# Performance work log

Measured on AMD Instinct MI355X. Metric: run time of the kernel, lower is better.

Reference implementation:

```python
import jax, jax.numpy as jnp
import numpy as np

NEG_SLOPE = 0.2  # PyG GATConv default leaky_relu slope


def gat_layer(x, src, dst, W, a_src, a_dst, bias, heads, d, concat):
    # x: [N, in_dim]; src/dst: [E] (edges flow src -> dst, self-loops included)
    N = x.shape[0]
    h = (x @ W).reshape(N, heads, d)                      # [N, H, D]
    alpha_src = jnp.einsum('nhd,hd->nh', h, a_src)        # [N, H]
    alpha_dst = jnp.einsum('nhd,hd->nh', h, a_dst)        # [N, H]
    e = jax.nn.leaky_relu(alpha_src[src] + alpha_dst[dst], NEG_SLOPE)  # [E, H]
    # softmax over incoming edges of each destination node (segment softmax)
    m = jax.ops.segment_max(e, dst, num_segments=N)       # [N, H]
    ex = jnp.exp(e - m[dst])
    s = jax.ops.segment_sum(ex, dst, num_segments=N)      # [N, H]
    alpha = ex / s[dst]                                   # [E, H]
    msg = h[src] * alpha[..., None]                       # [E, H, D]
    out = jax.ops.segment_sum(msg, dst, num_segments=N)   # [N, H, D]
    out = out.reshape(N, heads * d) if concat else out.mean(axis=1)
    return out + bias


def setup_inputs() -> dict:
    key = jax.random.key(0)
    ks = jax.random.split(key, 12)
    N, E = 10000, 320000
    in_dim, hidden, heads, out_dim = 256, 64, 4, 40
    x = jax.random.normal(ks[0], (N, in_dim), dtype=jnp.float32)
    edge_index = jax.random.randint(ks[1], (2, E), 0, N, dtype=jnp.int64)
    s = 0.1
    return {
        'x': x,
        'edge_index': edge_index,
        'W1': jax.random.normal(ks[2], (in_dim, heads * hidden), jnp.float32) * s,
        'att_src1': jax.random.normal(ks[3], (heads, hidden), jnp.float32) * s,
        'att_dst1': jax.random.normal(ks[4], (heads, hidden), jnp.float32) * s,
        'bias1': jnp.zeros((heads * hidden,), jnp.float32),
        'W2': jax.random.normal(ks[5], (heads * hidden, out_dim), jnp.float32) * s,
        'att_src2': jax.random.normal(ks[6], (1, out_dim), jnp.float32) * s,
        'att_dst2': jax.random.normal(ks[7], (1, out_dim), jnp.float32) * s,
        'bias2': jnp.zeros((out_dim,), jnp.float32),
    }


def reference(x, edge_index, W1, att_src1, att_dst1, bias1, W2, att_src2, att_dst2, bias2):
    N = x.shape[0]
    # PyG GATConv adds self-loops by default
    loop = jnp.arange(N, dtype=edge_index.dtype)
    src = jnp.concatenate([edge_index[0], loop])
    dst = jnp.concatenate([edge_index[1], loop])
    h = gat_layer(x, src, dst, W1, att_src1, att_dst1, bias1, heads=4, d=64, concat=True)
    h = jax.nn.relu(h)
    out = gat_layer(h, src, dst, W2, att_src2, att_dst2, bias2, heads=1, d=40, concat=False)
    return jax.nn.log_softmax(out, axis=1)
```

## Files before the change

kernel.cpp:

```cpp
#include <hip/hip_runtime.h>
#include <hip/hip_bf16.h>
#include <math.h>

#define IN_DIM 256
#define C1 256
#define H1 4
#define OUT_DIM 40
#define W2PAD 48
#define NEG_SLOPE 0.2f
#define DSTRIDE 128

typedef __attribute__((ext_vector_type(8))) short bf16x8;
typedef __attribute__((ext_vector_type(4))) float f32x4;
typedef __attribute__((ext_vector_type(2))) float f32x2;

#define XS_LD 264

__device__ __forceinline__ unsigned short f2bf(float f) {
    union { float f; unsigned u; } c; c.f = f;
    unsigned r = c.u + 0x7fffu + ((c.u >> 16) & 1u);
    return (unsigned short)(r >> 16);
}

__device__ __forceinline__ unsigned char f2fp8(float f) {
    return (unsigned char)__builtin_amdgcn_cvt_pk_fp8_f32(f, 0.f, 0, false);
}

__device__ __forceinline__ float sel4(float4 v, int h) {
    float r = v.x;
    r = (h == 1) ? v.y : r;
    r = (h == 2) ? v.z : r;
    r = (h == 3) ? v.w : r;
    return r;
}

__device__ __forceinline__ float leaky(float v) {
    return (v >= 0.0f) ? v : NEG_SLOPE * v;
}

__global__ void k_prep(int* __restrict__ fill, const float* __restrict__ W1,
                       unsigned short* __restrict__ W1t, const float* __restrict__ W2,
                       unsigned short* __restrict__ W2t, const float* __restrict__ a_src2,
                       const float* __restrict__ a_dst2, float* __restrict__ w2s,
                       float* __restrict__ w2d, int N) {
    int t = threadIdx.x;
    int g = blockIdx.x * 256 + t;
    if (g < N) fill[g << 4] = 0;
    if (g < C1) {
        float s = 0.0f, d = 0.0f;
#pragma unroll
        for (int j = 0; j < OUT_DIM; ++j) {
            float w = W2[g * OUT_DIM + j];
            s += w * a_src2[j];
            d += w * a_dst2[j];
        }
        w2s[g] = s;
        w2d[g] = d;
    }
    if (g < W2PAD * C1) {
        int j = g >> 8, k = g & 255;
        W2t[g] = (j < OUT_DIM) ? f2bf(W2[k * OUT_DIM + j]) : 0;
    }
    __shared__ float s32[32][33];
    int b = blockIdx.x;
    int r0 = (b >> 3) * 32;
    int c0 = (b & 7) * 32;
    for (int i = t; i < 1024; i += 256) {
        int lr = i >> 5, lc = i & 31;
        s32[lr][lc] = W1[(r0 + lr) * 256 + c0 + lc];
    }
    __syncthreads();
    for (int i = t; i < 1024; i += 256) {
        int oc = i >> 5, ok = i & 31;
        W1t[(c0 + oc) * 256 + r0 + ok] = f2bf(s32[ok][oc]);
    }
}

__global__ void __launch_bounds__(256) k_fused1(
    const float* __restrict__ x, const unsigned short* __restrict__ W1t,
    const float* __restrict__ a_src, const float* __restrict__ a_dst,
    unsigned char* __restrict__ h1, float* __restrict__ as1, float* __restrict__ ad1,
    const int* __restrict__ ei, int* __restrict__ fill, unsigned short* __restrict__ srcs,
    int N, int E, int ET, int G1) {
    __shared__ unsigned short xs[64 * XS_LD];
    int t = threadIdx.x;

    if (blockIdx.x >= G1) {
        int eb = (blockIdx.x - G1) * 1024 + t;
#pragma unroll
        for (int k = 0; k < 4; ++k) {
            int e = eb + k * 256;
            if (e < ET) {
                int s, d;
                if (e < E) { s = ei[e]; d = ei[E + e]; }
                else       { s = e - E; d = s; }
                int pos = atomicAdd(&fill[d << 4], 1);
                srcs[(d << 7) + pos] = (unsigned short)s;
            }
        }
        return;
    }

    int n0 = blockIdx.x * 64;
    for (int i = t; i < 4096; i += 256) {
        int r = i >> 6, c4 = i & 63;
        int n = n0 + r;
        float4 v = (n < N) ? ((const float4*)x)[(size_t)n * 64 + c4]
                           : make_float4(0.f, 0.f, 0.f, 0.f);
        uint2 pk;
        pk.x = (unsigned)f2bf(v.x) | ((unsigned)f2bf(v.y) << 16);
        pk.y = (unsigned)f2bf(v.z) | ((unsigned)f2bf(v.w) << 16);
        *((uint2*)&xs[r * XS_LD + c4 * 4]) = pk;
    }
    __syncthreads();

    int wv = t >> 6, lane = t & 63;
    int quad = lane >> 4, ln = lane & 15;

    f32x4 acc[4][4];
#pragma unroll
    for (int mt = 0; mt < 4; ++mt)
#pragma unroll
        for (int nt = 0; nt < 4; ++nt) acc[mt][nt] = (f32x4){0.f, 0.f, 0.f, 0.f};

#pragma unroll
    for (int kb = 0; kb < 8; ++kb) {
        bf16x8 af[4], bfv[4];
#pragma unroll
        for (int mt = 0; mt < 4; ++mt)
            af[mt] = *((bf16x8*)&xs[(mt * 16 + ln) * XS_LD + kb * 32 + quad * 8]);
#pragma unroll
        for (int nt = 0; nt < 4; ++nt)
            bfv[nt] = *((const bf16x8*)(W1t + ((wv * 64 + nt * 16 + ln) * 256 + kb * 32 + quad * 8)));
#pragma unroll
        for (int mt = 0; mt < 4; ++mt)
#pragma unroll
            for (int nt = 0; nt < 4; ++nt)
                acc[mt][nt] = __builtin_amdgcn_mfma_f32_16x16x32_bf16(af[mt], bfv[nt], acc[mt][nt], 0, 0, 0);
    }

    float asv[4], adv[4];
#pragma unroll
    for (int nt = 0; nt < 4; ++nt) {
        int col = wv * 64 + nt * 16 + ln;
        asv[nt] = a_src[col];
        adv[nt] = a_dst[col];
    }
#pragma unroll
    for (int mt = 0; mt < 4; ++mt) {
        float ds[4] = {0.f, 0.f, 0.f, 0.f};
        float dd[4] = {0.f, 0.f, 0.f, 0.f};
#pragma unroll
        for (int nt = 0; nt < 4; ++nt) {
#pragma unroll
            for (int r = 0; r < 4; ++r) {
                float v = acc[mt][nt][r];
                ds[r] += v * asv[nt];
                dd[r] += v * adv[nt];
            }
        }
#pragma unroll
        for (int r = 0; r < 4; ++r) {
            float vs = ds[r], vd = dd[r];
#pragma unroll
            for (int o = 1; o < 16; o <<= 1) {
                vs += __shfl_xor(vs, o);
                vd += __shfl_xor(vd, o);
            }
            if (ln == 0) {
                int node = n0 + mt * 16 + quad * 4 + r;
                if (node < N) {
                    as1[node * H1 + wv] = vs;
                    ad1[node * H1 + wv] = vd;
                }
            }
        }
    }

    __syncthreads();
    unsigned char* bt = (unsigned char*)xs;
#pragma unroll
    for (int mt = 0; mt < 4; ++mt)
#pragma unroll
        for (int nt = 0; nt < 4; ++nt)
#pragma unroll
            for (int r = 0; r < 4; ++r)
                bt[(mt * 16 + quad * 4 + r) * 256 + wv * 64 + nt * 16 + ln] = f2fp8(acc[mt][nt][r]);
    __syncthreads();
    const uint4* bt4 = (const uint4*)bt;
    uint4* h14 = (uint4*)(h1 + (size_t)n0 * C1);
    for (int i = t; i < 1024; i += 256) {
        int row = i >> 4;
        if (n0 + row < N) h14[i] = bt4[i];
    }
}

__global__ void __launch_bounds__(256) k_node1(
    const int* __restrict__ fill, const unsigned short* __restrict__ srcs,
    const float* __restrict__ as1f, const float* __restrict__ ad1f,
    const unsigned char* __restrict__ h1, const float* __restrict__ bias1,
    const float* __restrict__ w2s, const float* __restrict__ w2d,
    const unsigned short* __restrict__ W2t, unsigned short* __restrict__ h2b,
    float* __restrict__ as2, float* __restrict__ ad2, int N) {
    int w = threadIdx.x >> 6, lane = threadIdx.x & 63;
    int n = blockIdx.x * 4 + w;
    bool valid = (n < N);
    __shared__ float4 es[4][64];
    __shared__ unsigned short Abuf[16 * 256];
    int half = lane >> 5, hl = lane & 31;
    int h8 = hl >> 3;
    int start = n << 7;
    int end = start + (valid ? fill[n << 4] : 0);
    const float4* as4 = (const float4*)as1f;
    float4 adn = valid ? ((const float4*)ad1f)[n] : make_float4(0.f, 0.f, 0.f, 0.f);
    const float* esw = (const float*)&es[w][0];

    float4 S4 = make_float4(0.f, 0.f, 0.f, 0.f);
    float acc[8];
#pragma unroll
    for (int k = 0; k < 8; ++k) acc[k] = 0.f;

    for (int c = start; c < end; c += 64) {
        int cnt = min(64, end - c);
        int idx = c + lane;
        int sreg = (idx < end) ? (int)srcs[idx] : 0;
        float4 exv = make_float4(0.f, 0.f, 0.f, 0.f);
        if (idx < end) {
            float4 a = as4[sreg];
            exv.x = __expf(leaky(a.x + adn.x));
            exv.y = __expf(leaky(a.y + adn.y));
            exv.z = __expf(leaky(a.z + adn.z));
            exv.w = __expf(leaky(a.w + adn.w));
        }
        S4.x += exv.x; S4.y += exv.y; S4.z += exv.z; S4.w += exv.w;
        es[w][lane] = exv;

        int i = 0;
        for (; i + 15 < cnt; i += 16) {
            int s[8]; float a[8]; uint2 r[8];
#pragma unroll
            for (int k = 0; k < 8; ++k) {
                int j = i + 2 * k + half;
                s[k] = __shfl(sreg, j);
                a[k] = esw[j * 4 + h8];
            }
#pragma unroll
            for (int k = 0; k < 8; ++k)
                r[k] = *((const uint2*)(h1 + (size_t)s[k] * C1) + hl);
#pragma unroll
            for (int k = 0; k < 8; ++k) {
                f32x2 lo0 = __builtin_amdgcn_cvt_pk_f32_fp8(r[k].x, false);
                f32x2 hi0 = __builtin_amdgcn_cvt_pk_f32_fp8(r[k].x, true);
                f32x2 lo1 = __builtin_amdgcn_cvt_pk_f32_fp8(r[k].y, false);
                f32x2 hi1 = __builtin_amdgcn_cvt_pk_f32_fp8(r[k].y, true);
                acc[0] += a[k] * lo0.x; acc[1] += a[k] * lo0.y;
                acc[2] += a[k] * hi0.x; acc[3] += a[k] * hi0.y;
                acc[4] += a[k] * lo1.x; acc[5] += a[k] * lo1.y;
                acc[6] += a[k] * hi1.x; acc[7] += a[k] * hi1.y;
            }
        }
        for (; i + 7 < cnt; i += 8) {
            int s[4]; float a[4]; uint2 r[4];
#pragma unroll
            for (int k = 0; k < 4; ++k) {
                int j = i + 2 * k + half;
                s[k] = __shfl(sreg, j);
                a[k] = esw[j * 4 + h8];
            }
#pragma unroll
            for (int k = 0; k < 4; ++k)
                r[k] = *((const uint2*)(h1 + (size_t)s[k] * C1) + hl);
#pragma unroll
            for (int k = 0; k < 4; ++k) {
                f32x2 lo0 = __builtin_amdgcn_cvt_pk_f32_fp8(r[k].x, false);
                f32x2 hi0 = __builtin_amdgcn_cvt_pk_f32_fp8(r[k].x, true);
                f32x2 lo1 = __builtin_amdgcn_cvt_pk_f32_fp8(r[k].y, false);
                f32x2 hi1 = __builtin_amdgcn_cvt_pk_f32_fp8(r[k].y, true);
                acc[0] += a[k] * lo0.x; acc[1] += a[k] * lo0.y;
                acc[2] += a[k] * hi0.x; acc[3] += a[k] * hi0.y;
                acc[4] += a[k] * lo1.x; acc[5] += a[k] * lo1.y;
                acc[6] += a[k] * hi1.x; acc[7] += a[k] * hi1.y;
            }
        }
        for (; i < cnt; i += 2) {
            int j = i + half;
            int s0 = __shfl(sreg, j);
            float a0 = esw[j * 4 + h8];
            uint2 r0 = *((const uint2*)(h1 + (size_t)s0 * C1) + hl);
            f32x2 lo0 = __builtin_amdgcn_cvt_pk_f32_fp8(r0.x, false);
            f32x2 hi0 = __builtin_amdgcn_cvt_pk_f32_fp8(r0.x, true);
            f32x2 lo1 = __builtin_amdgcn_cvt_pk_f32_fp8(r0.y, false);
            f32x2 hi1 = __builtin_amdgcn_cvt_pk_f32_fp8(r0.y, true);
            acc[0] += a0 * lo0.x; acc[1] += a0 * lo0.y;
            acc[2] += a0 * hi0.x; acc[3] += a0 * hi0.y;
            acc[4] += a0 * lo1.x; acc[5] += a0 * lo1.y;
            acc[6] += a0 * hi1.x; acc[7] += a0 * hi1.y;
        }
    }

#pragma unroll
    for (int k = 0; k < 8; ++k) acc[k] += __shfl_xor(acc[k], 32);

#pragma unroll
    for (int o = 32; o > 0; o >>= 1) {
        S4.x += __shfl_xor(S4.x, o);
        S4.y += __shfl_xor(S4.y, o);
        S4.z += __shfl_xor(S4.z, o);
        S4.w += __shfl_xor(S4.w, o);
    }
    float iS = 1.0f / sel4(S4, h8);
    float4 b0 = ((const float4*)bias1)[hl * 2];
    float4 b1 = ((const float4*)bias1)[hl * 2 + 1];
    float v0 = fmaxf(acc[0] * iS + b0.x, 0.f);
    float v1 = fmaxf(acc[1] * iS + b0.y, 0.f);
    float v2 = fmaxf(acc[2] * iS + b0.z, 0.f);
    float v3 = fmaxf(acc[3] * iS + b0.w, 0.f);
    float v4 = fmaxf(acc[4] * iS + b1.x, 0.f);
    float v5 = fmaxf(acc[5] * iS + b1.y, 0.f);
    float v6 = fmaxf(acc[6] * iS + b1.z, 0.f);
    float v7 = fmaxf(acc[7] * iS + b1.w, 0.f);
    if (half == 0) {
        uint4 pk;
        pk.x = (unsigned)f2bf(v0) | ((unsigned)f2bf(v1) << 16);
        pk.y = (unsigned)f2bf(v2) | ((unsigned)f2bf(v3) << 16);
        pk.z = (unsigned)f2bf(v4) | ((unsigned)f2bf(v5) << 16);
        pk.w = (unsigned)f2bf(v6) | ((unsigned)f2bf(v7) << 16);
        ((uint4*)&Abuf[w * 256])[hl] = pk;
    }

    float4 ws0 = ((const float4*)w2s)[hl * 2];
    float4 ws1 = ((const float4*)w2s)[hl * 2 + 1];
    float4 wd0 = ((const float4*)w2d)[hl * 2];
    float4 wd1 = ((const float4*)w2d)[hl * 2 + 1];
    float ps = v0 * ws0.x + v1 * ws0.y + v2 * ws0.z + v3 * ws0.w
             + v4 * ws1.x + v5 * ws1.y + v6 * ws1.z + v7 * ws1.w;
    float pd = v0 * wd0.x + v1 * wd0.y + v2 * wd0.z + v3 * wd0.w
             + v4 * wd1.x + v5 * wd1.y + v6 * wd1.z + v7 * wd1.w;
#pragma unroll
    for (int o = 16; o > 0; o >>= 1) {
        ps += __shfl_xor(ps, o);
        pd += __shfl_xor(pd, o);
    }
    if (lane == 0 && valid) { as2[n] = ps; ad2[n] = pd; }

    __syncthreads();
    if (w < 3) {
        int quad = lane >> 4, ln = lane & 15;
        f32x4 accm = (f32x4){0.f, 0.f, 0.f, 0.f};
        const unsigned short* bbase = W2t + (w * 16 + ln) * 256;
#pragma unroll
        for (int kb = 0; kb < 8; ++kb) {
            bf16x8 af = *((bf16x8*)&Abuf[ln * 256 + kb * 32 + quad * 8]);
            bf16x8 bfr = *((const bf16x8*)(bbase + kb * 32 + quad * 8));
            accm = __builtin_amdgcn_mfma_f32_16x16x32_bf16(af, bfr, accm, 0, 0, 0);
        }
        int col = w * 16 + ln;
        if (col < OUT_DIM && quad == 0) {
#pragma unroll
            for (int r = 0; r < 4; ++r) {
                int node = blockIdx.x * 4 + r;
                if (node < N) h2b[(size_t)node * OUT_DIM + col] = f2bf(accm[r]);
            }
        }
    }
}

__global__ void __launch_bounds__(256) k_node2(
    const int* __restrict__ fill, const unsigned short* __restrict__ srcs,
    const float* __restrict__ as2, const float* __restrict__ ad2,
    const unsigned short* __restrict__ h2b, const float* __restrict__ bias2,
    float* __restrict__ out, int N) {
    int w = threadIdx.x >> 6, lane = threadIdx.x & 63;
    int n = blockIdx.x * 4 + w;
    if (n >= N) return;
    int g = lane / 10;
    int gl = lane - g * 10;
    int start = n << 7;
    int end = start + fill[n << 4];
    float adn = ad2[n];
    float S = 0.f;
    float acc0 = 0.f, acc1 = 0.f, acc2 = 0.f, acc3 = 0.f;

    for (int c = start; c < end; c += 64) {
        int cnt = min(64, end - c);
        int idx = c + lane;
        int sreg = (idx < end) ? (int)srcs[idx] : 0;
        float ex = (idx < end) ? __expf(leaky(as2[sreg] + adn)) : 0.f;
        S += ex;
        for (int i = 0; i < cnt; i += 24) {
            int j0 = i + g, j1 = i + 6 + g, j2 = i + 12 + g, j3 = i + 18 + g;
            int jc0 = min(j0, 63), jc1 = min(j1, 63), jc2 = min(j2, 63), jc3 = min(j3, 63);
            int su0 = __shfl(sreg, jc0), su1 = __shfl(sreg, jc1);
            int su2 = __shfl(sreg, jc2), su3 = __shfl(sreg, jc3);
            float al0 = __shfl(ex, jc0), al1 = __shfl(ex, jc1);
            float al2 = __shfl(ex, jc2), al3 = __shfl(ex, jc3);
            if (j0 >= cnt) al0 = 0.f;
            if (j1 >= cnt) al1 = 0.f;
            if (j2 >= cnt) al2 = 0.f;
            if (j3 >= cnt) al3 = 0.f;
            uint2 r0 = *((const uint2*)(h2b + (size_t)su0 * OUT_DIM) + gl);
            uint2 r1 = *((const uint2*)(h2b + (size_t)su1 * OUT_DIM) + gl);
            uint2 r2 = *((const uint2*)(h2b + (size_t)su2 * OUT_DIM) + gl);
            uint2 r3 = *((const uint2*)(h2b + (size_t)su3 * OUT_DIM) + gl);
            acc0 += al0 * __uint_as_float(r0.x << 16)         + al1 * __uint_as_float(r1.x << 16)
                  + al2 * __uint_as_float(r2.x << 16)         + al3 * __uint_as_float(r3.x << 16);
            acc1 += al0 * __uint_as_float(r0.x & 0xffff0000u) + al1 * __uint_as_float(r1.x & 0xffff0000u)
                  + al2 * __uint_as_float(r2.x & 0xffff0000u) + al3 * __uint_as_float(r3.x & 0xffff0000u);
            acc2 += al0 * __uint_as_float(r0.y << 16)         + al1 * __uint_as_float(r1.y << 16)
                  + al2 * __uint_as_float(r2.y << 16)         + al3 * __uint_as_float(r3.y << 16);
            acc3 += al0 * __uint_as_float(r0.y & 0xffff0000u) + al1 * __uint_as_float(r1.y & 0xffff0000u)
                  + al2 * __uint_as_float(r2.y & 0xffff0000u) + al3 * __uint_as_float(r3.y & 0xffff0000u);
        }
    }

    int l10 = min(lane + 10, 63), l20 = min(lane + 20, 63), l30 = min(lane + 30, 63);
    int l40 = min(lane + 40, 63), l50 = min(lane + 50, 63);
    float t0 = acc0 + __shfl(acc0, l10) + __shfl(acc0, l20) + __shfl(acc0, l30)
                    + __shfl(acc0, l40) + __shfl(acc0, l50);
    float t1 = acc1 + __shfl(acc1, l10) + __shfl(acc1, l20) + __shfl(acc1, l30)
                    + __shfl(acc1, l40) + __shfl(acc1, l50);
    float t2 = acc2 + __shfl(acc2, l10) + __shfl(acc2, l20) + __shfl(acc2, l30)
                    + __shfl(acc2, l40) + __shfl(acc2, l50);
    float t3 = acc3 + __shfl(acc3, l10) + __shfl(acc3, l20) + __shfl(acc3, l30)
                    + __shfl(acc3, l40) + __shfl(acc3, l50);
#pragma unroll
    for (int o = 32; o > 0; o >>= 1) S += __shfl_xor(S, o);

    bool act = lane < 10;
    float iS = 1.0f / S;
    float4 bz = make_float4(0.f, 0.f, 0.f, 0.f);
    if (act) bz = ((const float4*)bias2)[lane];
    float v0 = act ? (t0 * iS + bz.x) : -INFINITY;
    float v1 = act ? (t1 * iS + bz.y) : -INFINITY;
    float v2 = act ? (t2 * iS + bz.z) : -INFINITY;
    float v3 = act ? (t3 * iS + bz.w) : -INFINITY;
    float mx = fmaxf(fmaxf(v0, v1), fmaxf(v2, v3));
#pragma unroll
    for (int o = 8; o > 0; o >>= 1) mx = fmaxf(mx, __shfl_xor(mx, o));
    float e0 = act ? __expf(v0 - mx) : 0.f;
    float e1 = act ? __expf(v1 - mx) : 0.f;
    float e2 = act ? __expf(v2 - mx) : 0.f;
    float e3 = act ? __expf(v3 - mx) : 0.f;
    float esum = (e0 + e1) + (e2 + e3);
#pragma unroll
    for (int o = 8; o > 0; o >>= 1) esum += __shfl_xor(esum, o);
    if (act) {
        float l = mx + logf(esum);
        *((float4*)(out + (size_t)n * OUT_DIM) + lane) = make_float4(v0 - l, v1 - l, v2 - l, v3 - l);
    }
}

extern "C" void kernel_launch(void* const* d_in, const int* in_sizes, int n_in,
                              void* d_out, int out_size, void* d_ws, size_t ws_size,
                              hipStream_t stream) {
    const float* x        = (const float*)d_in[0];
    const int*   ei       = (const int*)d_in[1];
    const float* W1       = (const float*)d_in[2];
    const float* att_src1 = (const float*)d_in[3];
    const float* att_dst1 = (const float*)d_in[4];
    const float* bias1    = (const float*)d_in[5];
    const float* W2       = (const float*)d_in[6];
    const float* att_src2 = (const float*)d_in[7];
    const float* att_dst2 = (const float*)d_in[8];
    const float* bias2    = (const float*)d_in[9];
    float* out = (float*)d_out;

    const int N  = in_sizes[0] / IN_DIM;
    const int E  = in_sizes[1] / 2;
    const int ET = E + N;

    char* base = (char*)d_ws;
    auto alloc = [&](size_t bytes) {
        char* p = base;
        base += (bytes + 255) & ~(size_t)255;
        return p;
    };
    unsigned char*  h1    = (unsigned char*)alloc((size_t)N * C1);
    unsigned short* W1t   = (unsigned short*)alloc((size_t)C1 * C1 * 2);
    unsigned short* W2t   = (unsigned short*)alloc((size_t)W2PAD * C1 * 2);
    unsigned short* h2b   = (unsigned short*)alloc((size_t)N * OUT_DIM * 2);
    float* as1   = (float*)alloc((size_t)N * H1 * 4);
    float* ad1   = (float*)alloc((size_t)N * H1 * 4);
    float* as2   = (float*)alloc((size_t)N * 4);
    float* ad2   = (float*)alloc((size_t)N * 4);
    float* w2s   = (float*)alloc((size_t)C1 * 4);
    float* w2d   = (float*)alloc((size_t)C1 * 4);
    int* fill    = (int*)alloc((size_t)N * 16 * 4);
    unsigned short* srcs = (unsigned short*)alloc((size_t)N * DSTRIDE * 2);

    const int G1 = (N + 63) / 64;
    const int GS = (ET + 1023) / 1024;

    k_prep<<<64, 256, 0, stream>>>(fill, W1, W1t, W2, W2t, att_src2, att_dst2, w2s, w2d, N);
    k_fused1<<<G1 + GS, 256, 0, stream>>>(x, W1t, att_src1, att_dst1, h1, as1, ad1,
                                          ei, fill, srcs, N, E, ET, G1);
    k_node1<<<(N + 3) / 4, 256, 0, stream>>>(fill, srcs, as1, ad1, h1, bias1, w2s, w2d,
                                             W2t, h2b, as2, ad2, N);
    k_node2<<<(N + 3) / 4, 256, 0, stream>>>(fill, srcs, as2, ad2, h2b, bias2, out, N);
}
```

Baseline: 139.7 us.

## Write h1 directly in permuted fp8 layout and halve GEMM row tile

The GEMM kernel now packs four fp8 values per lane straight from MFMA accumulators and stores them to global memory. This drops the LDS staging transpose and its two barriers, at the cost of a permuted column order in h1. That permutation is absorbed downstream by reordering W2t, w2s/w2d and a new permuted bias1p in the prep kernel. The row tile per block shrinks from 64 to 32 nodes, roughly doubling the GEMM grid and reducing LDS per block, while each block reuses the W1 fragments over fewer rows.

```diff
diff --git a/kernel.cpp b/kernel.cpp
--- a/kernel.cpp
+++ b/kernel.cpp
@@ -15,15 +15,12 @@
 typedef __attribute__((ext_vector_type(2))) float f32x2;
 
 #define XS_LD 264
+#define MT 2
 
 __device__ __forceinline__ unsigned short f2bf(float f) {
     union { float f; unsigned u; } c; c.f = f;
     unsigned r = c.u + 0x7fffu + ((c.u >> 16) & 1u);
     return (unsigned short)(r >> 16);
-}
-
-__device__ __forceinline__ unsigned char f2fp8(float f) {
-    return (unsigned char)__builtin_amdgcn_cvt_pk_fp8_f32(f, 0.f, 0, false);
 }
 
 __device__ __forceinline__ float sel4(float4 v, int h) {
@@ -38,28 +35,35 @@
     return (v >= 0.0f) ? v : NEG_SLOPE * v;
 }
 
+__device__ __forceinline__ int permc(int B) {
+    return (B & 0xC0) + (B & 3) * 16 + ((B >> 2) & 15);
+}
+
 __global__ void k_prep(int* __restrict__ fill, const float* __restrict__ W1,
                        unsigned short* __restrict__ W1t, const float* __restrict__ W2,
                        unsigned short* __restrict__ W2t, const float* __restrict__ a_src2,
                        const float* __restrict__ a_dst2, float* __restrict__ w2s,
-                       float* __restrict__ w2d, int N) {
+                       float* __restrict__ w2d, const float* __restrict__ bias1,
+                       float* __restrict__ bias1p, int N) {
     int t = threadIdx.x;
     int g = blockIdx.x * 256 + t;
     if (g < N) fill[g << 4] = 0;
     if (g < C1) {
+        int c = permc(g);
         float s = 0.0f, d = 0.0f;
 #pragma unroll
         for (int j = 0; j < OUT_DIM; ++j) {
-            float w = W2[g * OUT_DIM + j];
+            float w = W2[c * OUT_DIM + j];
             s += w * a_src2[j];
             d += w * a_dst2[j];
         }
         w2s[g] = s;
         w2d[g] = d;
+        bias1p[g] = bias1[c];
     }
     if (g < W2PAD * C1) {
-        int j = g >> 8, k = g & 255;
-        W2t[g] = (j < OUT_DIM) ? f2bf(W2[k * OUT_DIM + j]) : 0;
+        int j = g >> 8, B = g & 255;
+        W2t[g] = (j < OUT_DIM) ? f2bf(W2[permc(B) * OUT_DIM + j]) : 0;
     }
     __shared__ float s32[32][33];
     int b = blockIdx.x;
@@ -82,7 +86,7 @@
     unsigned char* __restrict__ h1, float* __restrict__ as1, float* __restrict__ ad1,
     const int* __restrict__ ei, int* __restrict__ fill, unsigned short* __restrict__ srcs,
     int N, int E, int ET, int G1) {
-    __shared__ unsigned short xs[64 * XS_LD];
+    __shared__ unsigned short xs[32 * XS_LD];
     int t = threadIdx.x;
 
     if (blockIdx.x >= G1) {
@@ -101,8 +105,8 @@
         return;
     }
 
-    int n0 = blockIdx.x * 64;
-    for (int i = t; i < 4096; i += 256) {
+    int n0 = blockIdx.x * (MT * 16);
+    for (int i = t; i < 32 * 64; i += 256) {
         int r = i >> 6, c4 = i & 63;
         int n = n0 + r;
         float4 v = (n < N) ? ((const float4*)x)[(size_t)n * 64 + c4]
@@ -117,23 +121,23 @@
     int wv = t >> 6, lane = t & 63;
     int quad = lane >> 4, ln = lane & 15;
 
-    f32x4 acc[4][4];
-#pragma unroll
-    for (int mt = 0; mt < 4; ++mt)
+    f32x4 acc[MT][4];
+#pragma unroll
+    for (int mt = 0; mt < MT; ++mt)
 #pragma unroll
         for (int nt = 0; nt < 4; ++nt) acc[mt][nt] = (f32x4){0.f, 0.f, 0.f, 0.f};
 
 #pragma unroll
     for (int kb = 0; kb < 8; ++kb) {
-        bf16x8 af[4], bfv[4];
-#pragma unroll
-        for (int mt = 0; mt < 4; ++mt)
+        bf16x8 af[MT], bfv[4];
+#pragma unroll
+        for (int mt = 0; mt < MT; ++mt)
             af[mt] = *((bf16x8*)&xs[(mt * 16 + ln) * XS_LD + kb * 32 + quad * 8]);
 #pragma unroll
         for (int nt = 0; nt < 4; ++nt)
             bfv[nt] = *((const bf16x8*)(W1t + ((wv * 64 + nt * 16 + ln) * 256 + kb * 32 + quad * 8)));
 #pragma unroll
-        for (int mt = 0; mt < 4; ++mt)
+        for (int mt = 0; mt < MT; ++mt)
 #pragma unroll
             for (int nt = 0; nt < 4; ++nt)
                 acc[mt][nt] = __builtin_amdgcn_mfma_f32_16x16x32_bf16(af[mt], bfv[nt], acc[mt][nt], 0, 0, 0);
@@ -147,7 +151,7 @@
         adv[nt] = a_dst[col];
     }
 #pragma unroll
-    for (int mt = 0; mt < 4; ++mt) {
+    for (int mt = 0; mt < MT; ++mt) {
         float ds[4] = {0.f, 0.f, 0.f, 0.f};
         float dd[4] = {0.f, 0.f, 0.f, 0.f};
 #pragma unroll
@@ -177,28 +181,23 @@
         }
     }
 
-    __syncthreads();
-    unsigned char* bt = (unsigned char*)xs;
-#pragma unroll
-    for (int mt = 0; mt < 4; ++mt)
-#pragma unroll
-        for (int nt = 0; nt < 4; ++nt)
-#pragma unroll
-            for (int r = 0; r < 4; ++r)
-                bt[(mt * 16 + quad * 4 + r) * 256 + wv * 64 + nt * 16 + ln] = f2fp8(acc[mt][nt][r]);
-    __syncthreads();
-    const uint4* bt4 = (const uint4*)bt;
-    uint4* h14 = (uint4*)(h1 + (size_t)n0 * C1);
-    for (int i = t; i < 1024; i += 256) {
-        int row = i >> 4;
-        if (n0 + row < N) h14[i] = bt4[i];
+#pragma unroll
+    for (int mt = 0; mt < MT; ++mt) {
+#pragma unroll
+        for (int r = 0; r < 4; ++r) {
+            int row = n0 + mt * 16 + quad * 4 + r;
+            unsigned d = (unsigned)__builtin_amdgcn_cvt_pk_fp8_f32(acc[mt][0][r], acc[mt][1][r], 0, false);
+            d = (unsigned)__builtin_amdgcn_cvt_pk_fp8_f32(acc[mt][2][r], acc[mt][3][r], d, true);
+            if (row < N)
+                *(unsigned*)(h1 + (size_t)row * C1 + wv * 64 + ln * 4) = d;
+        }
     }
 }
 
 __global__ void __launch_bounds__(256) k_node1(
     const int* __restrict__ fill, const unsigned short* __restrict__ srcs,
     const float* __restrict__ as1f, const float* __restrict__ ad1f,
-    const unsigned char* __restrict__ h1, const float* __restrict__ bias1,
+    const unsigned char* __restrict__ h1, const float* __restrict__ bias1p,
     const float* __restrict__ w2s, const float* __restrict__ w2d,
     const unsigned short* __restrict__ W2t, unsigned short* __restrict__ h2b,
     float* __restrict__ as2, float* __restrict__ ad2, int N) {
@@ -309,8 +308,8 @@
         S4.w += __shfl_xor(S4.w, o);
     }
     float iS = 1.0f / sel4(S4, h8);
-    float4 b0 = ((const float4*)bias1)[hl * 2];
-    float4 b1 = ((const float4*)bias1)[hl * 2 + 1];
+    float4 b0 = ((const float4*)bias1p)[hl * 2];
+    float4 b1 = ((const float4*)bias1p)[hl * 2 + 1];
     float v0 = fmaxf(acc[0] * iS + b0.x, 0.f);
     float v1 = fmaxf(acc[1] * iS + b0.y, 0.f);
     float v2 = fmaxf(acc[2] * iS + b0.z, 0.f);
@@ -479,22 +478,24 @@
     unsigned short* W1t   = (unsigned short*)alloc((size_t)C1 * C1 * 2);
     unsigned short* W2t   = (unsigned short*)alloc((size_t)W2PAD * C1 * 2);
     unsigned short* h2b   = (unsigned short*)alloc((size_t)N * OUT_DIM * 2);
-    float* as1   = (float*)alloc((size_t)N * H1 * 4);
-    float* ad1   = (float*)alloc((size_t)N * H1 * 4);
-    float* as2   = (float*)alloc((size_t)N * 4);
-    float* ad2   = (float*)alloc((size_t)N * 4);
-    float* w2s   = (float*)alloc((size_t)C1 * 4);
-    float* w2d   = (float*)alloc((size_t)C1 * 4);
-    int* fill    = (int*)alloc((size_t)N * 16 * 4);
+    float* as1    = (float*)alloc((size_t)N * H1 * 4);
+    float* ad1    = (float*)alloc((size_t)N * H1 * 4);
+    float* as2    = (float*)alloc((size_t)N * 4);
+    float* ad2    = (float*)alloc((size_t)N * 4);
+    float* w2s    = (float*)alloc((size_t)C1 * 4);
+    float* w2d    = (float*)alloc((size_t)C1 * 4);
+    float* bias1p = (float*)alloc((size_t)C1 * 4);
+    int* fill     = (int*)alloc((size_t)N * 16 * 4);
     unsigned short* srcs = (unsigned short*)alloc((size_t)N * DSTRIDE * 2);
 
-    const int G1 = (N + 63) / 64;
+    const int G1 = (N + MT * 16 - 1) / (MT * 16);
     const int GS = (ET + 1023) / 1024;
 
-    k_prep<<<64, 256, 0, stream>>>(fill, W1, W1t, W2, W2t, att_src2, att_dst2, w2s, w2d, N);
+    k_prep<<<64, 256, 0, stream>>>(fill, W1, W1t, W2, W2t, att_src2, att_dst2, w2s, w2d,
+                                   bias1, bias1p, N);
     k_fused1<<<G1 + GS, 256, 0, stream>>>(x, W1t, att_src1, att_dst1, h1, as1, ad1,
                                           ei, fill, srcs, N, E, ET, G1);
-    k_node1<<<(N + 3) / 4, 256, 0, stream>>>(fill, srcs, as1, ad1, h1, bias1, w2s, w2d,
+    k_node1<<<(N + 3) / 4, 256, 0, stream>>>(fill, srcs, as1, ad1, h1, bias1p, w2s, w2d,
                                              W2t, h2b, as2, ad2, N);
     k_node2<<<(N + 3) / 4, 256, 0, stream>>>(fill, srcs, as2, ad2, h2b, bias2, out, N);
 }
```

Measured after the change: 135.1 us. 3.3% less time.
